# Kernel optimization log

Hardware: AMD Instinct MI355X
Metric: run time of the kernel (lower is better)

Reference implementation:

```python
import jax, jax.numpy as jnp
import numpy as np

B, N, D, H = 256, 32768, 1024, 16
DH = D // H

def setup_inputs() -> dict:
    key = jax.random.key(0)
    ks = jax.random.split(key, 6)
    scale = 1.0 / np.sqrt(D)  # xavier-ish scale for weights
    return {
        "q": jax.random.normal(ks[0], (B, D), jnp.float32),
        "k": jax.random.normal(ks[1], (N, D), jnp.float32),
        "v": jax.random.normal(ks[2], (N, D), jnp.float32),
        "W_q": jax.random.normal(ks[3], (D, D), jnp.float32) * scale,
        "W_k": jax.random.normal(ks[4], (D, D), jnp.float32) * scale,
        "W_v": jax.random.normal(ks[5], (D, D), jnp.float32) * scale,
    }

def reference(q, k, v, W_q, W_k, W_v):
    # nn.Linear(x) = x @ W.T (no bias)
    qh = (q @ W_q.T).reshape(B, H, DH)   # [B,H,dh]
    kh = (k @ W_k.T).reshape(N, H, DH)   # [N,H,dh]
    vh = (v @ W_v.T).reshape(N, H, DH)   # [N,H,dh]
    inv_sqrt_dh = 1.0 / np.sqrt(DH).astype(np.float32)
    # decode-style cross attention: single query per (head, batch) over N keys
    score = jnp.einsum('bhd,nhd->hbn', qh, kh) * inv_sqrt_dh  # [H,B,N]
    weights = jax.nn.softmax(score, axis=-1)                   # [H,B,N]
    # dropout is identity in eval mode
    context = jnp.einsum('hbn,nhd->bhd', weights, vh)          # [B,H,dh]
    return context.reshape(B, D)
```

## Files before the change

### kernel.cpp

```cpp
#include <hip/hip_runtime.h>
#include <hip/hip_bf16.h>

#define B_  256
#define N_  32768
#define D_  1024
#define H_  16
#define DH_ 64
#define KSPLIT 32
#define STRIPE (N_ / KSPLIT)

typedef __attribute__((ext_vector_type(8))) short bf16x8;
typedef __attribute__((ext_vector_type(4))) float f32x4;

static __device__ __forceinline__ short f2bf(float f) {
    union { __hip_bfloat16 h; short s; } u;
    u.h = __float2bfloat16(f);
    return u.s;
}

static __device__ __forceinline__ bf16x8 pack8(float4 a, float4 b) {
    bf16x8 r;
    r[0] = f2bf(a.x); r[1] = f2bf(a.y); r[2] = f2bf(a.z); r[3] = f2bf(a.w);
    r[4] = f2bf(b.x); r[5] = f2bf(b.y); r[6] = f2bf(b.z); r[7] = f2bf(b.w);
    return r;
}

static __device__ __forceinline__ void gload16(const void* g, void* l) {
    __builtin_amdgcn_global_load_lds(
        (const __attribute__((address_space(1))) void*)g,
        (__attribute__((address_space(3))) void*)l, 16, 0, 0);
}

__global__ __launch_bounds__(256)
void f2b_kernel(const float* __restrict__ in, short* __restrict__ out, int n4)
{
    int i = blockIdx.x * 256 + threadIdx.x;
    if (i < n4) {
        float4 v = ((const float4*)in)[i];
        ((short4*)out)[i] = make_short4(f2bf(v.x), f2bf(v.y), f2bf(v.z), f2bf(v.w));
    }
}

template<bool SWAP>
__global__ __launch_bounds__(256, 2)
void gemm_hybrid(const float* __restrict__ P, const short* __restrict__ Qb,
                 short* __restrict__ C, int MP, int MQ, int K, int ldc, float alpha)
{
    __shared__ __align__(16) float Pf[128 * 32];
    __shared__ __align__(16) short Qs[128 * 32];

    const int tid  = threadIdx.x;
    const int wave = tid >> 6;
    const int lane = tid & 63;
    const int quad = lane >> 4;
    const int l16  = lane & 15;

    const int gp = MP >> 7, gq = MQ >> 7;
    const int bid = blockIdx.x;
    int bp, bq;
    if (gp >= 8) {
        int xcd = bid & 7, w = bid >> 3, sp = gp >> 3;
        bp = xcd * sp + w / gq;
        bq = w % gq;
    } else { bp = bid / gq; bq = bid % gq; }

    const int wm = (wave & 1) * 64;
    const int wn = (wave >> 1) * 64;

    const char* gA[4]; char* lA[4];
#pragma unroll
    for (int j = 0; j < 4; ++j) {
        int s = j * 256 + tid;
        int r = s >> 3;
        int c = (s & 7) ^ (r & 7);
        gA[j] = (const char*)(P + (size_t)(bp * 128 + r) * K) + c * 16;
        lA[j] = (char*)Pf + s * 16;
    }
    const char* gW[2]; char* lW[2];
#pragma unroll
    for (int j = 0; j < 2; ++j) {
        int s = j * 256 + tid;
        int r = s >> 2;
        int c = (s & 3) ^ ((r >> 1) & 3);
        gW[j] = (const char*)(Qb + (size_t)(bq * 128 + r) * K) + c * 16;
        lW[j] = (char*)Qs + s * 16;
    }

    const int rowPf0 = SWAP ? wn : wm;
    const int rowQs0 = SWAP ? wm : wn;
    int offPf[4][2], offQs[4];
#pragma unroll
    for (int f = 0; f < 4; ++f) {
        int r = rowPf0 + f * 16 + l16;
        offPf[f][0] = (r * 8 + ((quad * 2)     ^ (r & 7))) * 16;
        offPf[f][1] = (r * 8 + ((quad * 2 + 1) ^ (r & 7))) * 16;
        int r2 = rowQs0 + f * 16 + l16;
        offQs[f] = (r2 * 4 + (quad ^ ((r2 >> 1) & 3))) * 16;
    }

    f32x4 acc[4][4];
#pragma unroll
    for (int i = 0; i < 4; ++i)
#pragma unroll
        for (int j = 0; j < 4; ++j) acc[i][j] = (f32x4){0.f, 0.f, 0.f, 0.f};

    for (int kt = 0; kt < K; kt += 32) {
        __syncthreads();
#pragma unroll
        for (int j = 0; j < 4; ++j) { gload16(gA[j], lA[j]); gA[j] += 128; }
#pragma unroll
        for (int j = 0; j < 2; ++j) { gload16(gW[j], lW[j]); gW[j] += 64; }
        __syncthreads();

        bf16x8 fp[4], fq[4];
#pragma unroll
        for (int f = 0; f < 4; ++f) {
            float4 a = *(const float4*)((const char*)Pf + offPf[f][0]);
            float4 b = *(const float4*)((const char*)Pf + offPf[f][1]);
            fp[f] = pack8(a, b);
            fq[f] = *(const bf16x8*)((const char*)Qs + offQs[f]);
        }
#pragma unroll
        for (int mi = 0; mi < 4; ++mi)
#pragma unroll
            for (int ni = 0; ni < 4; ++ni)
                acc[mi][ni] = __builtin_amdgcn_mfma_f32_16x16x32_bf16(
                    SWAP ? fq[mi] : fp[mi], SWAP ? fp[ni] : fq[ni],
                    acc[mi][ni], 0, 0, 0);
    }

    const int rb = (SWAP ? bq : bp) * 128;
    const int cb = (SWAP ? bp : bq) * 128;
#pragma unroll
    for (int mi = 0; mi < 4; ++mi)
#pragma unroll
        for (int ni = 0; ni < 4; ++ni)
#pragma unroll
            for (int reg = 0; reg < 4; ++reg) {
                int r = rb + wm + mi * 16 + quad * 4 + reg;
                int c = cb + wn + ni * 16 + l16;
                C[(size_t)r * ldc + c] = f2bf(acc[mi][ni][reg] * alpha);
            }
}

__global__ __launch_bounds__(256, 2)
void attn_kernel(const short* __restrict__ qh, const short* __restrict__ kh,
                 const short* __restrict__ vhT, float* __restrict__ partO,
                 float* __restrict__ partM, float* __restrict__ partL)
{
    const int st = blockIdx.x, qb2 = blockIdx.y, h = blockIdx.z;
    const int tid  = threadIdx.x;
    const int wave = tid >> 6;
    const int lane = tid & 63;
    const int quad = lane >> 4;
    const int l16  = lane & 15;

    __shared__ __align__(16) short Ps[4][32][72];

    const int qbase = qb2 * 128 + wave * 32;
    const int hoff  = h * DH_;

    bf16x8 qfr[2][2];
#pragma unroll
    for (int qf = 0; qf < 2; ++qf)
#pragma unroll
        for (int ks = 0; ks < 2; ++ks)
            qfr[qf][ks] = *(const bf16x8*)(qh + (size_t)(qbase + qf * 16 + l16) * D_
                                           + hoff + ks * 32 + quad * 8);

    f32x4 ofrag[2][4];
#pragma unroll
    for (int qf = 0; qf < 2; ++qf)
#pragma unroll
        for (int dt = 0; dt < 4; ++dt) ofrag[qf][dt] = (f32x4){0.f, 0.f, 0.f, 0.f};
    float m_i[2] = {-__builtin_inff(), -__builtin_inff()};
    float l_i[2] = {0.f, 0.f};

    const int n0 = st * STRIPE;

    bf16x8 akf[4][2];
#pragma unroll
    for (int kf = 0; kf < 4; ++kf)
#pragma unroll
        for (int ks = 0; ks < 2; ++ks)
            akf[kf][ks] = *(const bf16x8*)(kh + (size_t)(n0 + kf * 16 + l16) * D_
                                           + hoff + ks * 32 + quad * 8);

    for (int ch = 0; ch < STRIPE; ch += 64) {
        const int nb = n0 + ch;

        f32x4 sf[4][2];
#pragma unroll
        for (int kf = 0; kf < 4; ++kf)
#pragma unroll
            for (int qf = 0; qf < 2; ++qf) sf[kf][qf] = (f32x4){0.f, 0.f, 0.f, 0.f};
#pragma unroll
        for (int ks = 0; ks < 2; ++ks)
#pragma unroll
            for (int kf = 0; kf < 4; ++kf)
#pragma unroll
                for (int qf = 0; qf < 2; ++qf)
                    sf[kf][qf] = __builtin_amdgcn_mfma_f32_16x16x32_bf16(
                        akf[kf][ks], qfr[qf][ks], sf[kf][qf], 0, 0, 0);

        bf16x8 avf[4][2];
#pragma unroll
        for (int dt = 0; dt < 4; ++dt)
#pragma unroll
            for (int g = 0; g < 2; ++g)
                avf[dt][g] = *(const bf16x8*)(vhT + (size_t)(hoff + dt * 16 + l16) * N_
                                              + nb + g * 32 + quad * 8);

        const int nbn = (ch + 64 < STRIPE) ? nb + 64 : nb;
#pragma unroll
        for (int kf = 0; kf < 4; ++kf)
#pragma unroll
            for (int ks = 0; ks < 2; ++ks)
                akf[kf][ks] = *(const bf16x8*)(kh + (size_t)(nbn + kf * 16 + l16) * D_
                                               + hoff + ks * 32 + quad * 8);

#pragma unroll
        for (int qf = 0; qf < 2; ++qf) {
            float mx = sf[0][qf][0];
#pragma unroll
            for (int kf = 0; kf < 4; ++kf)
#pragma unroll
                for (int r = 0; r < 4; ++r) mx = fmaxf(mx, sf[kf][qf][r]);
            mx = fmaxf(mx, __shfl_xor(mx, 16));
            mx = fmaxf(mx, __shfl_xor(mx, 32));
            float mn = fmaxf(m_i[qf], mx);
            float al = exp2f(m_i[qf] - mn);
            m_i[qf] = mn;
            float ps = 0.f;
#pragma unroll
            for (int kf = 0; kf < 4; ++kf) {
                float p0 = exp2f(sf[kf][qf][0] - mn);
                float p1 = exp2f(sf[kf][qf][1] - mn);
                float p2 = exp2f(sf[kf][qf][2] - mn);
                float p3 = exp2f(sf[kf][qf][3] - mn);
                ps += (p0 + p1) + (p2 + p3);
                *(short4*)&Ps[wave][qf * 16 + l16][kf * 16 + quad * 4] =
                    make_short4(f2bf(p0), f2bf(p1), f2bf(p2), f2bf(p3));
            }
            ps += __shfl_xor(ps, 16);
            ps += __shfl_xor(ps, 32);
            l_i[qf] = l_i[qf] * al + ps;
#pragma unroll
            for (int dt = 0; dt < 4; ++dt) ofrag[qf][dt] *= al;
        }

#pragma unroll
        for (int qf = 0; qf < 2; ++qf)
#pragma unroll
            for (int g = 0; g < 2; ++g) {
                bf16x8 bP = *(const bf16x8*)&Ps[wave][qf * 16 + l16][g * 32 + quad * 8];
#pragma unroll
                for (int dt = 0; dt < 4; ++dt)
                    ofrag[qf][dt] = __builtin_amdgcn_mfma_f32_16x16x32_bf16(
                        avf[dt][g], bP, ofrag[qf][dt], 0, 0, 0);
            }
    }

    const int pid = ((h * KSPLIT + st) * 2 + qb2) * 4 + wave;
#pragma unroll
    for (int qf = 0; qf < 2; ++qf)
#pragma unroll
        for (int dt = 0; dt < 4; ++dt)
            *(f32x4*)&partO[((size_t)pid * 32 + qf * 16 + l16) * 64 + dt * 16 + quad * 4]
                = ofrag[qf][dt];
    if (quad == 0) {
#pragma unroll
        for (int qf = 0; qf < 2; ++qf) {
            partM[pid * 32 + qf * 16 + l16] = m_i[qf];
            partL[pid * 32 + qf * 16 + l16] = l_i[qf];
        }
    }
}

__global__ __launch_bounds__(256)
void merge_kernel(const float* __restrict__ partO, const float* __restrict__ partM,
                  const float* __restrict__ partL, float* __restrict__ out)
{
    int idx = blockIdx.x * 256 + threadIdx.x;
    int b   = idx >> 10;
    int col = idx & 1023;
    int h   = col >> 6;
    int d   = col & 63;
    int blk32 = b >> 5, rin = b & 31;
    int qb2 = blk32 >> 2, w = blk32 & 3;

    float mmax = -__builtin_inff();
#pragma unroll
    for (int st = 0; st < KSPLIT; ++st) {
        int pid = ((h * KSPLIT + st) * 2 + qb2) * 4 + w;
        mmax = fmaxf(mmax, partM[pid * 32 + rin]);
    }
    float L = 0.f, o = 0.f;
#pragma unroll
    for (int st = 0; st < KSPLIT; ++st) {
        int pid = ((h * KSPLIT + st) * 2 + qb2) * 4 + w;
        float c = exp2f(partM[pid * 32 + rin] - mmax);
        L += c * partL[pid * 32 + rin];
        o += c * partO[((size_t)pid * 32 + rin) * 64 + d];
    }
    out[idx] = o / L;
}

extern "C" void kernel_launch(void* const* d_in, const int* in_sizes, int n_in,
                              void* d_out, int out_size, void* d_ws, size_t ws_size,
                              hipStream_t stream) {
    const float* q   = (const float*)d_in[0];
    const float* k   = (const float*)d_in[1];
    const float* v   = (const float*)d_in[2];
    const float* W_q = (const float*)d_in[3];
    const float* W_k = (const float*)d_in[4];
    const float* W_v = (const float*)d_in[5];
    float* out = (float*)d_out;

    short* qh  = (short*)d_ws;
    short* kh  = qh  + (size_t)B_ * D_;
    short* vhT = kh  + (size_t)N_ * D_;
    short* Wqb = vhT + (size_t)D_ * N_;
    short* Wkb = Wqb + (size_t)D_ * D_;
    short* Wvb = Wkb + (size_t)D_ * D_;
    float* partO = (float*)(Wvb + (size_t)D_ * D_);
    float* partM = partO + (size_t)4096 * 32 * 64;
    float* partL = partM + (size_t)4096 * 32;

    dim3 blk(256);
    const int w4 = (D_ * D_) / 4;
    const float alpha_q = 0.125f * 1.4426950408889634f;

    f2b_kernel<<<dim3(w4 / 256), blk, 0, stream>>>(W_q, Wqb, w4);
    f2b_kernel<<<dim3(w4 / 256), blk, 0, stream>>>(W_k, Wkb, w4);
    f2b_kernel<<<dim3(w4 / 256), blk, 0, stream>>>(W_v, Wvb, w4);

    gemm_hybrid<false><<<dim3(2 * 8), blk, 0, stream>>>(q, Wqb, qh, B_, D_, D_, D_, alpha_q);
    gemm_hybrid<false><<<dim3(256 * 8), blk, 0, stream>>>(k, Wkb, kh, N_, D_, D_, D_, 1.0f);
    gemm_hybrid<true><<<dim3(256 * 8), blk, 0, stream>>>(v, Wvb, vhT, N_, D_, D_, N_, 1.0f);

    attn_kernel<<<dim3(KSPLIT, 2, H_), blk, 0, stream>>>(qh, kh, vhT, partO, partM, partL);
    merge_kernel<<<dim3((B_ * D_) / 256), blk, 0, stream>>>(partO, partM, partL, out);
}
```

Before: 694.5 us.

## Pre-convert inputs to bf16 and share K/V loads across query blocks

Adds separate fp32-to-bf16 conversion passes for q, k and v, so the projection GEMMs load bf16 tiles for both operands instead of fp32 activation tiles converted per tile. The attention kernel now handles both query halves in one block, loading each K/V chunk once and reusing it for 256 queries. This trades an extra full conversion pass and halved attention grid parallelism for lower GEMM and attention memory traffic. The LDS swizzle was removed, which may add bank conflicts.

Measured after the change: 600.2 us. -13.6%, faster.

```diff
diff --git a/kernel.cpp b/kernel.cpp
--- a/kernel.cpp
+++ b/kernel.cpp
@@ -32,22 +32,23 @@
 }
 
 __global__ __launch_bounds__(256)
-void f2b_kernel(const float* __restrict__ in, short* __restrict__ out, int n4)
+void f2b_kernel(const float* __restrict__ in, short* __restrict__ out, int n8)
 {
     int i = blockIdx.x * 256 + threadIdx.x;
-    if (i < n4) {
-        float4 v = ((const float4*)in)[i];
-        ((short4*)out)[i] = make_short4(f2bf(v.x), f2bf(v.y), f2bf(v.z), f2bf(v.w));
+    if (i < n8) {
+        float4 a = ((const float4*)in)[2 * i];
+        float4 b = ((const float4*)in)[2 * i + 1];
+        ((bf16x8*)out)[i] = pack8(a, b);
     }
 }
 
 template<bool SWAP>
 __global__ __launch_bounds__(256, 2)
-void gemm_hybrid(const float* __restrict__ P, const short* __restrict__ Qb,
-                 short* __restrict__ C, int MP, int MQ, int K, int ldc, float alpha)
+void gemm_bb(const short* __restrict__ P, const short* __restrict__ Qb,
+             short* __restrict__ C, int MP, int MQ, int K, int ldc, float alpha)
 {
-    __shared__ __align__(16) float Pf[128 * 32];
-    __shared__ __align__(16) short Qs[128 * 32];
+    __shared__ __align__(16) short Ps_[128 * 32];
+    __shared__ __align__(16) short Qs_[128 * 32];
 
     const int tid  = threadIdx.x;
     const int wave = tid >> 6;
@@ -67,36 +68,20 @@
     const int wm = (wave & 1) * 64;
     const int wn = (wave >> 1) * 64;
 
-    const char* gA[4]; char* lA[4];
-#pragma unroll
-    for (int j = 0; j < 4; ++j) {
-        int s = j * 256 + tid;
-        int r = s >> 3;
-        int c = (s & 7) ^ (r & 7);
-        gA[j] = (const char*)(P + (size_t)(bp * 128 + r) * K) + c * 16;
-        lA[j] = (char*)Pf + s * 16;
-    }
+    const char* gP[2]; char* lP[2];
     const char* gW[2]; char* lW[2];
 #pragma unroll
     for (int j = 0; j < 2; ++j) {
         int s = j * 256 + tid;
-        int r = s >> 2;
-        int c = (s & 3) ^ ((r >> 1) & 3);
-        gW[j] = (const char*)(Qb + (size_t)(bq * 128 + r) * K) + c * 16;
-        lW[j] = (char*)Qs + s * 16;
-    }
-
-    const int rowPf0 = SWAP ? wn : wm;
-    const int rowQs0 = SWAP ? wm : wn;
-    int offPf[4][2], offQs[4];
-#pragma unroll
-    for (int f = 0; f < 4; ++f) {
-        int r = rowPf0 + f * 16 + l16;
-        offPf[f][0] = (r * 8 + ((quad * 2)     ^ (r & 7))) * 16;
-        offPf[f][1] = (r * 8 + ((quad * 2 + 1) ^ (r & 7))) * 16;
-        int r2 = rowQs0 + f * 16 + l16;
-        offQs[f] = (r2 * 4 + (quad ^ ((r2 >> 1) & 3))) * 16;
-    }
+        int r = s >> 2, g = s & 3;
+        gP[j] = (const char*)(P + (size_t)(bp * 128 + r) * K) + g * 16;
+        lP[j] = (char*)Ps_ + s * 16;
+        gW[j] = (const char*)(Qb + (size_t)(bq * 128 + r) * K) + g * 16;
+        lW[j] = (char*)Qs_ + s * 16;
+    }
+
+    const short* tileA = SWAP ? Qs_ : Ps_;
+    const short* tileB = SWAP ? Ps_ : Qs_;
 
     f32x4 acc[4][4];
 #pragma unroll
@@ -107,26 +92,24 @@
     for (int kt = 0; kt < K; kt += 32) {
         __syncthreads();
 #pragma unroll
-        for (int j = 0; j < 4; ++j) { gload16(gA[j], lA[j]); gA[j] += 128; }
-#pragma unroll
-        for (int j = 0; j < 2; ++j) { gload16(gW[j], lW[j]); gW[j] += 64; }
+        for (int j = 0; j < 2; ++j) {
+            gload16(gP[j], lP[j]); gP[j] += 64;
+            gload16(gW[j], lW[j]); gW[j] += 64;
+        }
         __syncthreads();
 
-        bf16x8 fp[4], fq[4];
+        bf16x8 af[4], bf[4];
 #pragma unroll
         for (int f = 0; f < 4; ++f) {
-            float4 a = *(const float4*)((const char*)Pf + offPf[f][0]);
-            float4 b = *(const float4*)((const char*)Pf + offPf[f][1]);
-            fp[f] = pack8(a, b);
-            fq[f] = *(const bf16x8*)((const char*)Qs + offQs[f]);
+            af[f] = *(const bf16x8*)&tileA[(wm + f * 16 + l16) * 32 + quad * 8];
+            bf[f] = *(const bf16x8*)&tileB[(wn + f * 16 + l16) * 32 + quad * 8];
         }
 #pragma unroll
         for (int mi = 0; mi < 4; ++mi)
 #pragma unroll
             for (int ni = 0; ni < 4; ++ni)
                 acc[mi][ni] = __builtin_amdgcn_mfma_f32_16x16x32_bf16(
-                    SWAP ? fq[mi] : fp[mi], SWAP ? fp[ni] : fq[ni],
-                    acc[mi][ni], 0, 0, 0);
+                    af[mi], bf[ni], acc[mi][ni], 0, 0, 0);
     }
 
     const int rb = (SWAP ? bq : bp) * 128;
@@ -148,7 +131,7 @@
                  const short* __restrict__ vhT, float* __restrict__ partO,
                  float* __restrict__ partM, float* __restrict__ partL)
 {
-    const int st = blockIdx.x, qb2 = blockIdx.y, h = blockIdx.z;
+    const int st = blockIdx.x, h = blockIdx.y;
     const int tid  = threadIdx.x;
     const int wave = tid >> 6;
     const int lane = tid & 63;
@@ -157,53 +140,43 @@
 
     __shared__ __align__(16) short Ps[4][32][72];
 
-    const int qbase = qb2 * 128 + wave * 32;
-    const int hoff  = h * DH_;
-
-    bf16x8 qfr[2][2];
-#pragma unroll
-    for (int qf = 0; qf < 2; ++qf)
-#pragma unroll
-        for (int ks = 0; ks < 2; ++ks)
-            qfr[qf][ks] = *(const bf16x8*)(qh + (size_t)(qbase + qf * 16 + l16) * D_
-                                           + hoff + ks * 32 + quad * 8);
-
-    f32x4 ofrag[2][4];
-#pragma unroll
-    for (int qf = 0; qf < 2; ++qf)
-#pragma unroll
-        for (int dt = 0; dt < 4; ++dt) ofrag[qf][dt] = (f32x4){0.f, 0.f, 0.f, 0.f};
-    float m_i[2] = {-__builtin_inff(), -__builtin_inff()};
-    float l_i[2] = {0.f, 0.f};
+    const int hoff = h * DH_;
+
+    bf16x8 qfr[2][2][2];
+#pragma unroll
+    for (int qb2 = 0; qb2 < 2; ++qb2)
+#pragma unroll
+        for (int qf = 0; qf < 2; ++qf)
+#pragma unroll
+            for (int ks = 0; ks < 2; ++ks)
+                qfr[qb2][qf][ks] = *(const bf16x8*)
+                    (qh + (size_t)(qb2 * 128 + wave * 32 + qf * 16 + l16) * D_
+                        + hoff + ks * 32 + quad * 8);
+
+    f32x4 ofrag[2][2][4];
+    float m_i[2][2], l_i[2][2];
+#pragma unroll
+    for (int qb2 = 0; qb2 < 2; ++qb2)
+#pragma unroll
+        for (int qf = 0; qf < 2; ++qf) {
+            m_i[qb2][qf] = -__builtin_inff();
+            l_i[qb2][qf] = 0.f;
+#pragma unroll
+            for (int dt = 0; dt < 4; ++dt) ofrag[qb2][qf][dt] = (f32x4){0.f,0.f,0.f,0.f};
+        }
 
     const int n0 = st * STRIPE;
-
-    bf16x8 akf[4][2];
-#pragma unroll
-    for (int kf = 0; kf < 4; ++kf)
-#pragma unroll
-        for (int ks = 0; ks < 2; ++ks)
-            akf[kf][ks] = *(const bf16x8*)(kh + (size_t)(n0 + kf * 16 + l16) * D_
-                                           + hoff + ks * 32 + quad * 8);
 
     for (int ch = 0; ch < STRIPE; ch += 64) {
         const int nb = n0 + ch;
 
-        f32x4 sf[4][2];
+        bf16x8 akf[4][2], avf[4][2];
 #pragma unroll
         for (int kf = 0; kf < 4; ++kf)
 #pragma unroll
-            for (int qf = 0; qf < 2; ++qf) sf[kf][qf] = (f32x4){0.f, 0.f, 0.f, 0.f};
-#pragma unroll
-        for (int ks = 0; ks < 2; ++ks)
-#pragma unroll
-            for (int kf = 0; kf < 4; ++kf)
-#pragma unroll
-                for (int qf = 0; qf < 2; ++qf)
-                    sf[kf][qf] = __builtin_amdgcn_mfma_f32_16x16x32_bf16(
-                        akf[kf][ks], qfr[qf][ks], sf[kf][qf], 0, 0, 0);
-
-        bf16x8 avf[4][2];
+            for (int ks = 0; ks < 2; ++ks)
+                akf[kf][ks] = *(const bf16x8*)(kh + (size_t)(nb + kf * 16 + l16) * D_
+                                               + hoff + ks * 32 + quad * 8);
 #pragma unroll
         for (int dt = 0; dt < 4; ++dt)
 #pragma unroll
@@ -211,69 +184,81 @@
                 avf[dt][g] = *(const bf16x8*)(vhT + (size_t)(hoff + dt * 16 + l16) * N_
                                               + nb + g * 32 + quad * 8);
 
-        const int nbn = (ch + 64 < STRIPE) ? nb + 64 : nb;
-#pragma unroll
-        for (int kf = 0; kf < 4; ++kf)
+#pragma unroll
+        for (int qb2 = 0; qb2 < 2; ++qb2) {
+            f32x4 sf[4][2];
+#pragma unroll
+            for (int kf = 0; kf < 4; ++kf)
+#pragma unroll
+                for (int qf = 0; qf < 2; ++qf) sf[kf][qf] = (f32x4){0.f,0.f,0.f,0.f};
 #pragma unroll
             for (int ks = 0; ks < 2; ++ks)
-                akf[kf][ks] = *(const bf16x8*)(kh + (size_t)(nbn + kf * 16 + l16) * D_
-                                               + hoff + ks * 32 + quad * 8);
-
-#pragma unroll
-        for (int qf = 0; qf < 2; ++qf) {
-            float mx = sf[0][qf][0];
-#pragma unroll
-            for (int kf = 0; kf < 4; ++kf)
-#pragma unroll
-                for (int r = 0; r < 4; ++r) mx = fmaxf(mx, sf[kf][qf][r]);
-            mx = fmaxf(mx, __shfl_xor(mx, 16));
-            mx = fmaxf(mx, __shfl_xor(mx, 32));
-            float mn = fmaxf(m_i[qf], mx);
-            float al = exp2f(m_i[qf] - mn);
-            m_i[qf] = mn;
-            float ps = 0.f;
-#pragma unroll
-            for (int kf = 0; kf < 4; ++kf) {
-                float p0 = exp2f(sf[kf][qf][0] - mn);
-                float p1 = exp2f(sf[kf][qf][1] - mn);
-                float p2 = exp2f(sf[kf][qf][2] - mn);
-                float p3 = exp2f(sf[kf][qf][3] - mn);
-                ps += (p0 + p1) + (p2 + p3);
-                *(short4*)&Ps[wave][qf * 16 + l16][kf * 16 + quad * 4] =
-                    make_short4(f2bf(p0), f2bf(p1), f2bf(p2), f2bf(p3));
+#pragma unroll
+                for (int kf = 0; kf < 4; ++kf)
+#pragma unroll
+                    for (int qf = 0; qf < 2; ++qf)
+                        sf[kf][qf] = __builtin_amdgcn_mfma_f32_16x16x32_bf16(
+                            akf[kf][ks], qfr[qb2][qf][ks], sf[kf][qf], 0, 0, 0);
+
+#pragma unroll
+            for (int qf = 0; qf < 2; ++qf) {
+                float mx = sf[0][qf][0];
+#pragma unroll
+                for (int kf = 0; kf < 4; ++kf)
+#pragma unroll
+                    for (int r = 0; r < 4; ++r) mx = fmaxf(mx, sf[kf][qf][r]);
+                mx = fmaxf(mx, __shfl_xor(mx, 16));
+                mx = fmaxf(mx, __shfl_xor(mx, 32));
+                float mn = fmaxf(m_i[qb2][qf], mx);
+                float al = exp2f(m_i[qb2][qf] - mn);
+                m_i[qb2][qf] = mn;
+                float ps = 0.f;
+#pragma unroll
+                for (int kf = 0; kf < 4; ++kf) {
+                    float p0 = exp2f(sf[kf][qf][0] - mn);
+                    float p1 = exp2f(sf[kf][qf][1] - mn);
+                    float p2 = exp2f(sf[kf][qf][2] - mn);
+                    float p3 = exp2f(sf[kf][qf][3] - mn);
+                    ps += (p0 + p1) + (p2 + p3);
+                    *(short4*)&Ps[wave][qf * 16 + l16][kf * 16 + quad * 4] =
+                        make_short4(f2bf(p0), f2bf(p1), f2bf(p2), f2bf(p3));
+                }
+                ps += __shfl_xor(ps, 16);
+                ps += __shfl_xor(ps, 32);
+                l_i[qb2][qf] = l_i[qb2][qf] * al + ps;
+#pragma unroll
+                for (int dt = 0; dt < 4; ++dt) ofrag[qb2][qf][dt] *= al;
             }
-            ps += __shfl_xor(ps, 16);
-            ps += __shfl_xor(ps, 32);
-            l_i[qf] = l_i[qf] * al + ps;
-#pragma unroll
-            for (int dt = 0; dt < 4; ++dt) ofrag[qf][dt] *= al;
+
+#pragma unroll
+            for (int qf = 0; qf < 2; ++qf)
+#pragma unroll
+                for (int g = 0; g < 2; ++g) {
+                    bf16x8 bP = *(const bf16x8*)&Ps[wave][qf * 16 + l16][g * 32 + quad * 8];
+#pragma unroll
+                    for (int dt = 0; dt < 4; ++dt)
+                        ofrag[qb2][qf][dt] = __builtin_amdgcn_mfma_f32_16x16x32_bf16(
+                            avf[dt][g], bP, ofrag[qb2][qf][dt], 0, 0, 0);
+                }
         }
-
+    }
+
+    const int pid = (h * KSPLIT + st) * 4 + wave;
+#pragma unroll
+    for (int qb2 = 0; qb2 < 2; ++qb2) {
+        const size_t rowb = (size_t)(pid * 2 + qb2) * 32;
 #pragma unroll
         for (int qf = 0; qf < 2; ++qf)
 #pragma unroll
-            for (int g = 0; g < 2; ++g) {
-                bf16x8 bP = *(const bf16x8*)&Ps[wave][qf * 16 + l16][g * 32 + quad * 8];
-#pragma unroll
-                for (int dt = 0; dt < 4; ++dt)
-                    ofrag[qf][dt] = __builtin_amdgcn_mfma_f32_16x16x32_bf16(
-                        avf[dt][g], bP, ofrag[qf][dt], 0, 0, 0);
+            for (int dt = 0; dt < 4; ++dt)
+                *(f32x4*)&partO[(rowb + qf * 16 + l16) * 64 + dt * 16 + quad * 4]
+                    = ofrag[qb2][qf][dt];
+        if (quad == 0)
+#pragma unroll
+            for (int qf = 0; qf < 2; ++qf) {
+                partM[rowb + qf * 16 + l16] = m_i[qb2][qf];
+                partL[rowb + qf * 16 + l16] = l_i[qb2][qf];
             }
-    }
-
-    const int pid = ((h * KSPLIT + st) * 2 + qb2) * 4 + wave;
-#pragma unroll
-    for (int qf = 0; qf < 2; ++qf)
-#pragma unroll
-        for (int dt = 0; dt < 4; ++dt)
-            *(f32x4*)&partO[((size_t)pid * 32 + qf * 16 + l16) * 64 + dt * 16 + quad * 4]
-                = ofrag[qf][dt];
-    if (quad == 0) {
-#pragma unroll
-        for (int qf = 0; qf < 2; ++qf) {
-            partM[pid * 32 + qf * 16 + l16] = m_i[qf];
-            partL[pid * 32 + qf * 16 + l16] = l_i[qf];
-        }
     }
 }
 
@@ -286,22 +271,22 @@
     int col = idx & 1023;
     int h   = col >> 6;
     int d   = col & 63;
-    int blk32 = b >> 5, rin = b & 31;
-    int qb2 = blk32 >> 2, w = blk32 & 3;
+    int qb2 = b >> 7, rr = b & 127;
+    int w = rr >> 5, rin = rr & 31;
 
     float mmax = -__builtin_inff();
 #pragma unroll
     for (int st = 0; st < KSPLIT; ++st) {
-        int pid = ((h * KSPLIT + st) * 2 + qb2) * 4 + w;
-        mmax = fmaxf(mmax, partM[pid * 32 + rin]);
+        int slot = (((h * KSPLIT + st) * 4 + w) * 2 + qb2) * 32 + rin;
+        mmax = fmaxf(mmax, partM[slot]);
     }
     float L = 0.f, o = 0.f;
 #pragma unroll
     for (int st = 0; st < KSPLIT; ++st) {
-        int pid = ((h * KSPLIT + st) * 2 + qb2) * 4 + w;
-        float c = exp2f(partM[pid * 32 + rin] - mmax);
-        L += c * partL[pid * 32 + rin];
-        o += c * partO[((size_t)pid * 32 + rin) * 64 + d];
+        int slot = (((h * KSPLIT + st) * 4 + w) * 2 + qb2) * 32 + rin;
+        float c = exp2f(partM[slot] - mmax);
+        L += c * partL[slot];
+        o += c * partO[(size_t)slot * 64 + d];
     }
     out[idx] = o / L;
 }
@@ -320,7 +305,9 @@
     short* qh  = (short*)d_ws;
     short* kh  = qh  + (size_t)B_ * D_;
     short* vhT = kh  + (size_t)N_ * D_;
-    short* Wqb = vhT + (size_t)D_ * N_;
+    short* kvb = vhT + (size_t)D_ * N_;
+    short* qb  = kvb + (size_t)N_ * D_;
+    short* Wqb = qb  + (size_t)B_ * D_;
     short* Wkb = Wqb + (size_t)D_ * D_;
     short* Wvb = Wkb + (size_t)D_ * D_;
     float* partO = (float*)(Wvb + (size_t)D_ * D_);
@@ -328,17 +315,24 @@
     float* partL = partM + (size_t)4096 * 32;
 
     dim3 blk(256);
-    const int w4 = (D_ * D_) / 4;
+    const int w8  = (D_ * D_) / 8;
+    const int kv8 = (N_ * D_) / 8;
+    const int q8  = (B_ * D_) / 8;
     const float alpha_q = 0.125f * 1.4426950408889634f;
 
-    f2b_kernel<<<dim3(w4 / 256), blk, 0, stream>>>(W_q, Wqb, w4);
-    f2b_kernel<<<dim3(w4 / 256), blk, 0, stream>>>(W_k, Wkb, w4);
-    f2b_kernel<<<dim3(w4 / 256), blk, 0, stream>>>(W_v, Wvb, w4);
-
-    gemm_hybrid<false><<<dim3(2 * 8), blk, 0, stream>>>(q, Wqb, qh, B_, D_, D_, D_, alpha_q);
-    gemm_hybrid<false><<<dim3(256 * 8), blk, 0, stream>>>(k, Wkb, kh, N_, D_, D_, D_, 1.0f);
-    gemm_hybrid<true><<<dim3(256 * 8), blk, 0, stream>>>(v, Wvb, vhT, N_, D_, D_, N_, 1.0f);
-
-    attn_kernel<<<dim3(KSPLIT, 2, H_), blk, 0, stream>>>(qh, kh, vhT, partO, partM, partL);
+    f2b_kernel<<<dim3(w8 / 256), blk, 0, stream>>>(W_q, Wqb, w8);
+    f2b_kernel<<<dim3(w8 / 256), blk, 0, stream>>>(W_k, Wkb, w8);
+    f2b_kernel<<<dim3(w8 / 256), blk, 0, stream>>>(W_v, Wvb, w8);
+    f2b_kernel<<<dim3(q8 / 256), blk, 0, stream>>>(q, qb, q8);
+
+    gemm_bb<false><<<dim3(2 * 8), blk, 0, stream>>>(qb, Wqb, qh, B_, D_, D_, D_, alpha_q);
+
+    f2b_kernel<<<dim3(kv8 / 256), blk, 0, stream>>>(k, kvb, kv8);
+    gemm_bb<false><<<dim3(256 * 8), blk, 0, stream>>>(kvb, Wkb, kh, N_, D_, D_, D_, 1.0f);
+
+    f2b_kernel<<<dim3(kv8 / 256), blk, 0, stream>>>(v, kvb, kv8);
+    gemm_bb<true><<<dim3(256 * 8), blk, 0, stream>>>(kvb, Wvb, vhT, N_, D_, D_, N_, 1.0f);
+
+    attn_kernel<<<dim3(KSPLIT, H_), blk, 0, stream>>>(qh, kh, vhT, partO, partM, partL);
     merge_kernel<<<dim3((B_ * D_) / 256), blk, 0, stream>>>(partO, partM, partL, out);
 }
```
